# Kernel tuning notes

Measured on AMD Instinct MI355X. Metric: run time of the kernel, lower is better.

The kernel has to match this reference:

```python
import jax, jax.numpy as jnp
import numpy as np

N_NODES = 100000
N_EDGES = 1600000
NFEAT, NHID, NCLASS = 64, 128, 32


def _glorot(key, shape):
    fan_in, fan_out = shape[0], shape[1]
    lim = np.sqrt(6.0 / (fan_in + fan_out))
    return jax.random.uniform(key, shape, jnp.float32, -lim, lim)


def setup_inputs() -> dict:
    key = jax.random.key(0)
    ks = jax.random.split(key, 12)
    x = jax.random.normal(ks[0], (N_NODES, NFEAT), jnp.float32)
    edge_idx = jax.random.randint(ks[1], (2, N_EDGES), 0, N_NODES, jnp.int64)
    edge_weight = jax.random.uniform(ks[2], (N_EDGES,), jnp.float32)
    return {
        "x": x,
        "edge_idx": edge_idx,
        "edge_weight": edge_weight,
        # SAGEConv 1: out = mean_agg(x) @ Wl1 + b1 + x @ Wr1
        "Wl1": _glorot(ks[3], (NFEAT, NHID)),
        "Wr1": _glorot(ks[4], (NFEAT, NHID)),
        "b1": jnp.zeros((NHID,), jnp.float32),
        # SAGEConv 2
        "Wl2": _glorot(ks[5], (NHID, NHID)),
        "Wr2": _glorot(ks[6], (NHID, NHID)),
        "b2": jnp.zeros((NHID,), jnp.float32),
        # fc head: Linear(nhid, nclass) -> Linear(nclass, 1)
        "Wfc1": _glorot(ks[7], (NHID, NCLASS)),
        "bfc1": jnp.zeros((NCLASS,), jnp.float32),
        "Wfc2": _glorot(ks[8], (NCLASS, 1)),
        "bfc2": jnp.zeros((1,), jnp.float32),
    }


def _sage_conv(x, src, dst, Wl, Wr, b, n_nodes):
    # mean aggregation of source features at destination nodes
    msg_sum = jax.ops.segment_sum(x[src], dst, num_segments=n_nodes)  # [N, d]
    deg = jax.ops.segment_sum(jnp.ones((src.shape[0], 1), x.dtype), dst,
                              num_segments=n_nodes)                    # [N, 1]
    mean = msg_sum / jnp.maximum(deg, 1.0)
    return mean @ Wl + b + x @ Wr


def reference(x, edge_idx, edge_weight, Wl1, Wr1, b1, Wl2, Wr2, b2,
              Wfc1, bfc1, Wfc2, bfc2):
    n_nodes = x.shape[0]
    src, dst = edge_idx[0], edge_idx[1]
    # dropout is identity in eval mode (training=False)
    h = _sage_conv(x, src, dst, Wl1, Wr1, b1, n_nodes)   # [N, nhid]
    h = _sage_conv(h, src, dst, Wl2, Wr2, b2, n_nodes)   # [N, nhid]
    h = h @ Wfc1 + bfc1                                   # [N, nclass]
    out = h @ Wfc2 + bfc2                                 # [N, 1]
    return out
```

## Files before the change

### kernel.cpp

```cpp
#include <hip/hip_runtime.h>

#define S_SHIFT 8
#define S_NODES 256
#define NBKT    400
#define CAP     5120
#define CHUNK   8192
#define NREP    8
#define FTH     512
#define NDOTS   160

__global__ __launch_bounds__(FTH) void fused_kernel(
    const float* __restrict__ x,
    const int* __restrict__ src, const int* __restrict__ dst,
    int E, int N, int B, int nscat,
    int* __restrict__ cursor, unsigned* __restrict__ bucket,
    const float* __restrict__ Wl1, const float* __restrict__ Wr1, const float* __restrict__ b1,
    const float* __restrict__ Wl2, const float* __restrict__ Wr2, const float* __restrict__ b2,
    const float* __restrict__ Wfc1, const float* __restrict__ bfc1,
    const float* __restrict__ Wfc2, const float* __restrict__ bfc2,
    float* __restrict__ ga, float2* __restrict__ gbc, float* __restrict__ c01)
{
    __shared__ int hist[NBKT], lbase[NBKT], lcur[NBKT];
    __shared__ float wv[192], uu[128], vl2[128], vr2[128], w2[32];
    int t = threadIdx.x;
    int l = t & 63;
    int w = t >> 6;

    if ((int)blockIdx.x < nscat) {
        int e0 = blockIdx.x * CHUNK;
        int cnt = E - e0; if (cnt > CHUNK) cnt = CHUNK;
        for (int i = t; i < B; i += FTH) hist[i] = 0;
        __syncthreads();
        for (int i = t; i < cnt; i += FTH)
            atomicAdd(&hist[dst[e0 + i] >> S_SHIFT], 1);
        __syncthreads();
        for (int i = t; i < B; i += FTH) {
            lcur[i] = 0;
            if (hist[i] > 0) lbase[i] = atomicAdd(&cursor[i], hist[i]);
        }
        __syncthreads();
        for (int i = t; i < cnt; i += FTH) {
            int d = dst[e0 + i], s = src[e0 + i];
            int bb = d >> S_SHIFT;
            int off = atomicAdd(&lcur[bb], 1);
            bucket[(size_t)bb * CAP + (unsigned)(lbase[bb] + off)] =
                ((unsigned)s << S_SHIFT) | (unsigned)(d & (S_NODES - 1));
        }
    } else {
        if (t < 32) w2[t] = Wfc2[t];
        __syncthreads();
        for (int j = 0; j < 16; ++j) {
            int i = w + 8 * j;
            float p = (l < 32) ? Wfc1[i * 32 + l] * w2[l] : 0.f;
            for (int m = 16; m; m >>= 1) p += __shfl_xor(p, m);
            if (l == 0) uu[i] = p;
        }
        __syncthreads();
        for (int j = 0; j < 16; ++j) {
            int i = w + 8 * j;
            float ua = uu[l], ub = uu[64 + l];
            float pa = Wl2[i * 128 + l] * ua + Wl2[i * 128 + 64 + l] * ub;
            float pb = Wr2[i * 128 + l] * ua + Wr2[i * 128 + 64 + l] * ub;
            for (int m = 32; m; m >>= 1) { pa += __shfl_xor(pa, m); pb += __shfl_xor(pb, m); }
            if (l == 0) { vl2[i] = pa; vr2[i] = pb; }
        }
        __syncthreads();
        for (int j = 0; j < 8; ++j) {
            int i = w + 8 * j;
            float l1a = Wl1[i * 128 + l], l1b = Wl1[i * 128 + 64 + l];
            float r1a = Wr1[i * 128 + l], r1b = Wr1[i * 128 + 64 + l];
            float La = vl2[l], Lb = vl2[64 + l], Ra = vr2[l], Rb = vr2[64 + l];
            float pc = l1a * La + l1b * Lb;
            float pb = l1a * Ra + l1b * Rb + r1a * La + r1b * Lb;
            float pa = r1a * Ra + r1b * Rb;
            for (int m = 32; m; m >>= 1) {
                pa += __shfl_xor(pa, m); pb += __shfl_xor(pb, m); pc += __shfl_xor(pc, m);
            }
            if (l == 0) { wv[i] = pa; wv[64 + i] = pb; wv[128 + i] = pc; }
        }
        if ((int)blockIdx.x == nscat && w == 7) {
            float p0 = b1[l] * vr2[l] + b1[64 + l] * vr2[64 + l]
                     + b2[l] * uu[l] + b2[64 + l] * uu[64 + l];
            if (l < 32) p0 += bfc1[l] * w2[l];
            float p1 = b1[l] * vl2[l] + b1[64 + l] * vl2[64 + l];
            for (int m = 32; m; m >>= 1) { p0 += __shfl_xor(p0, m); p1 += __shfl_xor(p1, m); }
            if (l == 0) { c01[0] = p0 + bfc2[0]; c01[1] = p1; }
        }
        __syncthreads();

        int fp = l & 15, sub = l >> 4;
        float4 wa4 = ((const float4*)wv)[fp];
        float4 wb4 = ((const float4*)wv)[16 + fp];
        float4 wc4 = ((const float4*)wv)[32 + fp];
        const float4* x4 = (const float4*)x;
        int Q = (N + 3) >> 2;
        for (int qd = ((int)blockIdx.x - nscat) * 8 + w; qd < Q; qd += NDOTS * 8) {
            int node = qd * 4 + sub;
            float a = 0.f, b = 0.f, c = 0.f;
            if (node < N) {
                float4 v = x4[(size_t)node * 16 + fp];
                a = v.x * wa4.x + v.y * wa4.y + v.z * wa4.z + v.w * wa4.w;
                b = v.x * wb4.x + v.y * wb4.y + v.z * wb4.z + v.w * wb4.w;
                c = v.x * wc4.x + v.y * wc4.y + v.z * wc4.z + v.w * wc4.w;
            }
            for (int m = 8; m; m >>= 1) {
                a += __shfl_xor(a, m); b += __shfl_xor(b, m); c += __shfl_xor(c, m);
            }
            if (fp == 0 && node < N) { ga[node] = a; gbc[node] = make_float2(b, c); }
        }
    }
}

__global__ __launch_bounds__(512) void aggA_kernel(
    const unsigned* __restrict__ bucket, const int* __restrict__ cursor,
    const float2* __restrict__ gbc, const float* __restrict__ ga,
    const float* __restrict__ c01,
    float* __restrict__ q, float* __restrict__ t1, float* __restrict__ inv, int N)
{
    __shared__ float aB[NREP][S_NODES], aC[NREP][S_NODES];
    __shared__ int cnt[NREP][S_NODES];
    int t = threadIdx.x, b = blockIdx.x;
    int r = t >> 6;
    float* aBf = (float*)aB; float* aCf = (float*)aC; int* cnf = (int*)cnt;
    for (int i = t; i < NREP * S_NODES; i += 512) { aBf[i] = 0.f; aCf[i] = 0.f; cnf[i] = 0; }
    __syncthreads();
    int n = cursor[b];
    const unsigned* bp = bucket + (size_t)b * CAP;
    int n4 = n & ~3;
    for (int i = 4 * t; i < n4; i += 4 * 512) {
        uint4 e4 = *(const uint4*)(bp + i);
        float2 g0 = gbc[e4.x >> S_SHIFT];
        float2 g1 = gbc[e4.y >> S_SHIFT];
        float2 g2 = gbc[e4.z >> S_SHIFT];
        float2 g3 = gbc[e4.w >> S_SHIFT];
        int d0 = e4.x & (S_NODES - 1), d1 = e4.y & (S_NODES - 1);
        int d2 = e4.z & (S_NODES - 1), d3 = e4.w & (S_NODES - 1);
        atomicAdd(&aB[r][d0], g0.x); atomicAdd(&aC[r][d0], g0.y); atomicAdd(&cnt[r][d0], 1);
        atomicAdd(&aB[r][d1], g1.x); atomicAdd(&aC[r][d1], g1.y); atomicAdd(&cnt[r][d1], 1);
        atomicAdd(&aB[r][d2], g2.x); atomicAdd(&aC[r][d2], g2.y); atomicAdd(&cnt[r][d2], 1);
        atomicAdd(&aB[r][d3], g3.x); atomicAdd(&aC[r][d3], g3.y); atomicAdd(&cnt[r][d3], 1);
    }
    if (n4 + t < n) {
        unsigned uu = bp[n4 + t];
        float2 g = gbc[uu >> S_SHIFT];
        int dl = uu & (S_NODES - 1);
        atomicAdd(&aB[r][dl], g.x); atomicAdd(&aC[r][dl], g.y); atomicAdd(&cnt[r][dl], 1);
    }
    __syncthreads();
    if (t < S_NODES) {
        int node = (b << S_SHIFT) + t;
        if (node < N) {
            float sb = 0.f, sc = 0.f; int d = 0;
            #pragma unroll
            for (int k = 0; k < NREP; ++k) { sb += aB[k][t]; sc += aC[k][t]; d += cnt[k][t]; }
            float iv = 1.0f / ((d > 0) ? (float)d : 1.0f);
            inv[node] = iv;
            q[node]   = iv * sc;
            t1[node]  = ga[node] + iv * sb + c01[0] + (d > 0 ? c01[1] : 0.f);
        }
    }
}

__global__ __launch_bounds__(512) void aggB_kernel(
    const unsigned* __restrict__ bucket, const int* __restrict__ cursor,
    const float* __restrict__ q, const float* __restrict__ t1,
    const float* __restrict__ inv, float* __restrict__ out, int N)
{
    __shared__ float a2[NREP][S_NODES];
    int t = threadIdx.x, b = blockIdx.x;
    int r = t >> 6;
    float* a2f = (float*)a2;
    for (int i = t; i < NREP * S_NODES; i += 512) a2f[i] = 0.f;
    __syncthreads();
    int n = cursor[b];
    const unsigned* bp = bucket + (size_t)b * CAP;
    int n4 = n & ~3;
    for (int i = 4 * t; i < n4; i += 4 * 512) {
        uint4 e4 = *(const uint4*)(bp + i);
        float q0 = q[e4.x >> S_SHIFT], q1 = q[e4.y >> S_SHIFT];
        float q2 = q[e4.z >> S_SHIFT], q3 = q[e4.w >> S_SHIFT];
        atomicAdd(&a2[r][e4.x & (S_NODES - 1)], q0);
        atomicAdd(&a2[r][e4.y & (S_NODES - 1)], q1);
        atomicAdd(&a2[r][e4.z & (S_NODES - 1)], q2);
        atomicAdd(&a2[r][e4.w & (S_NODES - 1)], q3);
    }
    if (n4 + t < n) {
        unsigned uu = bp[n4 + t];
        atomicAdd(&a2[r][uu & (S_NODES - 1)], q[uu >> S_SHIFT]);
    }
    __syncthreads();
    if (t < S_NODES) {
        int node = (b << S_SHIFT) + t;
        if (node < N) {
            float s2 = 0.f;
            #pragma unroll
            for (int k = 0; k < NREP; ++k) s2 += a2[k][t];
            out[node] = t1[node] + inv[node] * s2;
        }
    }
}

extern "C" void kernel_launch(void* const* d_in, const int* in_sizes, int n_in,
                              void* d_out, int out_size, void* d_ws, size_t ws_size,
                              hipStream_t stream) {
    const float* x    = (const float*)d_in[0];
    const int*   eidx = (const int*)d_in[1];
    const float* Wl1  = (const float*)d_in[3];
    const float* Wr1  = (const float*)d_in[4];
    const float* b1   = (const float*)d_in[5];
    const float* Wl2  = (const float*)d_in[6];
    const float* Wr2  = (const float*)d_in[7];
    const float* b2   = (const float*)d_in[8];
    const float* Wfc1 = (const float*)d_in[9];
    const float* bfc1 = (const float*)d_in[10];
    const float* Wfc2 = (const float*)d_in[11];
    const float* bfc2 = (const float*)d_in[12];

    const int N = in_sizes[0] / 64;
    const int E = in_sizes[2];
    const int* src = eidx;
    const int* dst = eidx + E;
    const int B = (N + S_NODES - 1) / S_NODES;
    const int nscat = (E + CHUNK - 1) / CHUNK;

    char* ws = (char*)d_ws;
    int*      cursor = (int*)(ws);
    float*    c01    = (float*)(ws + 2048);
    float*    ga     = (float*)(ws + 4096);
    float*    q      = (float*)(ws + 4096 + (size_t)N * 4);
    float*    t1     = (float*)(ws + 4096 + (size_t)N * 8);
    float*    inv    = (float*)(ws + 4096 + (size_t)N * 12);
    float2*   gbc    = (float2*)(ws + 4096 + (size_t)N * 16);
    unsigned* bucket = (unsigned*)(ws + 4096 + (size_t)N * 24);

    hipMemsetAsync(cursor, 0, 2048, stream);

    fused_kernel<<<nscat + NDOTS, FTH, 0, stream>>>(
        x, src, dst, E, N, B, nscat, cursor, bucket,
        Wl1, Wr1, b1, Wl2, Wr2, b2, Wfc1, bfc1, Wfc2, bfc2,
        ga, gbc, c01);

    aggA_kernel<<<B, 512, 0, stream>>>(bucket, cursor, gbc, ga, c01, q, t1, inv, N);
    aggB_kernel<<<B, 512, 0, stream>>>(bucket, cursor, q, t1, inv, (float*)d_out, N);
}
```

Before: 168.7 us.

## Split weight folding into prep kernel and shrink buckets for more parallel blocks

Moves the weight-collapsing math and the cursor zeroing into a single-block prep kernel that writes folded vectors to global memory, replacing the memset and the redundant per-block recomputation in the dot blocks. The bucket granularity drops to 128 nodes, chunks to 4096 edges, replicas to 4, and blocks to 256 threads, so the scatter and aggregation grids have roughly twice as many blocks. The aim is better load balance and occupancy. The cost is an extra serial single-block launch and more global cursor atomics.

```diff
diff --git a/kernel.cpp b/kernel.cpp
--- a/kernel.cpp
+++ b/kernel.cpp
@@ -1,45 +1,97 @@
 #include <hip/hip_runtime.h>
 
-#define S_SHIFT 8
-#define S_NODES 256
-#define NBKT    400
-#define CAP     5120
-#define CHUNK   8192
-#define NREP    8
-#define FTH     512
-#define NDOTS   160
-
-__global__ __launch_bounds__(FTH) void fused_kernel(
-    const float* __restrict__ x,
-    const int* __restrict__ src, const int* __restrict__ dst,
-    int E, int N, int B, int nscat,
-    int* __restrict__ cursor, unsigned* __restrict__ bucket,
+#define S_SHIFT 7
+#define S_NODES 128
+#define NBKT    784
+#define CAP     2560
+#define CHUNK   4096
+#define NREP    4
+#define TPB     256
+#define TOTAL_BLOCKS 1024
+
+__global__ __launch_bounds__(512) void prep_kernel(
     const float* __restrict__ Wl1, const float* __restrict__ Wr1, const float* __restrict__ b1,
     const float* __restrict__ Wl2, const float* __restrict__ Wr2, const float* __restrict__ b2,
     const float* __restrict__ Wfc1, const float* __restrict__ bfc1,
     const float* __restrict__ Wfc2, const float* __restrict__ bfc2,
-    float* __restrict__ ga, float2* __restrict__ gbc, float* __restrict__ c01)
-{
-    __shared__ int hist[NBKT], lbase[NBKT], lcur[NBKT];
+    int* __restrict__ cursor, float* __restrict__ wv_g, float* __restrict__ c01)
+{
     __shared__ float wv[192], uu[128], vl2[128], vr2[128], w2[32];
     int t = threadIdx.x;
     int l = t & 63;
     int w = t >> 6;
-
-    if ((int)blockIdx.x < nscat) {
-        int e0 = blockIdx.x * CHUNK;
+    for (int i = t; i < NBKT; i += 512) cursor[i] = 0;
+    if (t < 32) w2[t] = Wfc2[t];
+    __syncthreads();
+    for (int j = 0; j < 16; ++j) {
+        int i = w + 8 * j;
+        float p = (l < 32) ? Wfc1[i * 32 + l] * w2[l] : 0.f;
+        for (int m = 16; m; m >>= 1) p += __shfl_xor(p, m);
+        if (l == 0) uu[i] = p;
+    }
+    __syncthreads();
+    for (int j = 0; j < 16; ++j) {
+        int i = w + 8 * j;
+        float ua = uu[l], ub = uu[64 + l];
+        float pa = Wl2[i * 128 + l] * ua + Wl2[i * 128 + 64 + l] * ub;
+        float pb = Wr2[i * 128 + l] * ua + Wr2[i * 128 + 64 + l] * ub;
+        for (int m = 32; m; m >>= 1) { pa += __shfl_xor(pa, m); pb += __shfl_xor(pb, m); }
+        if (l == 0) { vl2[i] = pa; vr2[i] = pb; }
+    }
+    __syncthreads();
+    for (int j = 0; j < 8; ++j) {
+        int i = w + 8 * j;
+        float l1a = Wl1[i * 128 + l], l1b = Wl1[i * 128 + 64 + l];
+        float r1a = Wr1[i * 128 + l], r1b = Wr1[i * 128 + 64 + l];
+        float La = vl2[l], Lb = vl2[64 + l], Ra = vr2[l], Rb = vr2[64 + l];
+        float pc = l1a * La + l1b * Lb;
+        float pb = l1a * Ra + l1b * Rb + r1a * La + r1b * Lb;
+        float pa = r1a * Ra + r1b * Rb;
+        for (int m = 32; m; m >>= 1) {
+            pa += __shfl_xor(pa, m); pb += __shfl_xor(pb, m); pc += __shfl_xor(pc, m);
+        }
+        if (l == 0) { wv[i] = pa; wv[64 + i] = pb; wv[128 + i] = pc; }
+    }
+    if (w == 7) {
+        float p0 = b1[l] * vr2[l] + b1[64 + l] * vr2[64 + l]
+                 + b2[l] * uu[l] + b2[64 + l] * uu[64 + l];
+        if (l < 32) p0 += bfc1[l] * w2[l];
+        float p1 = b1[l] * vl2[l] + b1[64 + l] * vl2[64 + l];
+        for (int m = 32; m; m >>= 1) { p0 += __shfl_xor(p0, m); p1 += __shfl_xor(p1, m); }
+        if (l == 0) { c01[0] = p0 + bfc2[0]; c01[1] = p1; }
+    }
+    __syncthreads();
+    for (int i = t; i < 192; i += 512) wv_g[i] = wv[i];
+}
+
+__global__ __launch_bounds__(TPB) void fused_kernel(
+    const float* __restrict__ x,
+    const int* __restrict__ src, const int* __restrict__ dst,
+    int E, int N, int B, int nscat, int ndot,
+    int* __restrict__ cursor, unsigned* __restrict__ bucket,
+    const float* __restrict__ wv_g,
+    float* __restrict__ ga, float2* __restrict__ gbc)
+{
+    __shared__ int hist[NBKT], lbase[NBKT], lcur[NBKT];
+    int t = threadIdx.x;
+    int l = t & 63;
+    int w = t >> 6;
+    int bid = blockIdx.x;
+
+    if (bid < nscat) {
+        int e0 = bid * CHUNK;
         int cnt = E - e0; if (cnt > CHUNK) cnt = CHUNK;
-        for (int i = t; i < B; i += FTH) hist[i] = 0;
+        for (int i = t; i < B; i += TPB) hist[i] = 0;
         __syncthreads();
-        for (int i = t; i < cnt; i += FTH)
+        for (int i = t; i < cnt; i += TPB)
             atomicAdd(&hist[dst[e0 + i] >> S_SHIFT], 1);
         __syncthreads();
-        for (int i = t; i < B; i += FTH) {
+        for (int i = t; i < B; i += TPB) {
             lcur[i] = 0;
             if (hist[i] > 0) lbase[i] = atomicAdd(&cursor[i], hist[i]);
         }
         __syncthreads();
-        for (int i = t; i < cnt; i += FTH) {
+        for (int i = t; i < cnt; i += TPB) {
             int d = dst[e0 + i], s = src[e0 + i];
             int bb = d >> S_SHIFT;
             int off = atomicAdd(&lcur[bb], 1);
@@ -47,54 +99,15 @@
                 ((unsigned)s << S_SHIFT) | (unsigned)(d & (S_NODES - 1));
         }
     } else {
-        if (t < 32) w2[t] = Wfc2[t];
-        __syncthreads();
-        for (int j = 0; j < 16; ++j) {
-            int i = w + 8 * j;
-            float p = (l < 32) ? Wfc1[i * 32 + l] * w2[l] : 0.f;
-            for (int m = 16; m; m >>= 1) p += __shfl_xor(p, m);
-            if (l == 0) uu[i] = p;
-        }
-        __syncthreads();
-        for (int j = 0; j < 16; ++j) {
-            int i = w + 8 * j;
-            float ua = uu[l], ub = uu[64 + l];
-            float pa = Wl2[i * 128 + l] * ua + Wl2[i * 128 + 64 + l] * ub;
-            float pb = Wr2[i * 128 + l] * ua + Wr2[i * 128 + 64 + l] * ub;
-            for (int m = 32; m; m >>= 1) { pa += __shfl_xor(pa, m); pb += __shfl_xor(pb, m); }
-            if (l == 0) { vl2[i] = pa; vr2[i] = pb; }
-        }
-        __syncthreads();
-        for (int j = 0; j < 8; ++j) {
-            int i = w + 8 * j;
-            float l1a = Wl1[i * 128 + l], l1b = Wl1[i * 128 + 64 + l];
-            float r1a = Wr1[i * 128 + l], r1b = Wr1[i * 128 + 64 + l];
-            float La = vl2[l], Lb = vl2[64 + l], Ra = vr2[l], Rb = vr2[64 + l];
-            float pc = l1a * La + l1b * Lb;
-            float pb = l1a * Ra + l1b * Rb + r1a * La + r1b * Lb;
-            float pa = r1a * Ra + r1b * Rb;
-            for (int m = 32; m; m >>= 1) {
-                pa += __shfl_xor(pa, m); pb += __shfl_xor(pb, m); pc += __shfl_xor(pc, m);
-            }
-            if (l == 0) { wv[i] = pa; wv[64 + i] = pb; wv[128 + i] = pc; }
-        }
-        if ((int)blockIdx.x == nscat && w == 7) {
-            float p0 = b1[l] * vr2[l] + b1[64 + l] * vr2[64 + l]
-                     + b2[l] * uu[l] + b2[64 + l] * uu[64 + l];
-            if (l < 32) p0 += bfc1[l] * w2[l];
-            float p1 = b1[l] * vl2[l] + b1[64 + l] * vl2[64 + l];
-            for (int m = 32; m; m >>= 1) { p0 += __shfl_xor(p0, m); p1 += __shfl_xor(p1, m); }
-            if (l == 0) { c01[0] = p0 + bfc2[0]; c01[1] = p1; }
-        }
-        __syncthreads();
-
         int fp = l & 15, sub = l >> 4;
-        float4 wa4 = ((const float4*)wv)[fp];
-        float4 wb4 = ((const float4*)wv)[16 + fp];
-        float4 wc4 = ((const float4*)wv)[32 + fp];
+        float4 wa4 = ((const float4*)wv_g)[fp];
+        float4 wb4 = ((const float4*)wv_g)[16 + fp];
+        float4 wc4 = ((const float4*)wv_g)[32 + fp];
         const float4* x4 = (const float4*)x;
         int Q = (N + 3) >> 2;
-        for (int qd = ((int)blockIdx.x - nscat) * 8 + w; qd < Q; qd += NDOTS * 8) {
+        int wid = (bid - nscat) * (TPB / 64) + w;
+        int stride = ndot * (TPB / 64);
+        for (int qd = wid; qd < Q; qd += stride) {
             int node = qd * 4 + sub;
             float a = 0.f, b = 0.f, c = 0.f;
             if (node < N) {
@@ -111,7 +124,7 @@
     }
 }
 
-__global__ __launch_bounds__(512) void aggA_kernel(
+__global__ __launch_bounds__(TPB) void aggA_kernel(
     const unsigned* __restrict__ bucket, const int* __restrict__ cursor,
     const float2* __restrict__ gbc, const float* __restrict__ ga,
     const float* __restrict__ c01,
@@ -122,12 +135,12 @@
     int t = threadIdx.x, b = blockIdx.x;
     int r = t >> 6;
     float* aBf = (float*)aB; float* aCf = (float*)aC; int* cnf = (int*)cnt;
-    for (int i = t; i < NREP * S_NODES; i += 512) { aBf[i] = 0.f; aCf[i] = 0.f; cnf[i] = 0; }
+    for (int i = t; i < NREP * S_NODES; i += TPB) { aBf[i] = 0.f; aCf[i] = 0.f; cnf[i] = 0; }
     __syncthreads();
     int n = cursor[b];
     const unsigned* bp = bucket + (size_t)b * CAP;
     int n4 = n & ~3;
-    for (int i = 4 * t; i < n4; i += 4 * 512) {
+    for (int i = 4 * t; i < n4; i += 4 * TPB) {
         uint4 e4 = *(const uint4*)(bp + i);
         float2 g0 = gbc[e4.x >> S_SHIFT];
         float2 g1 = gbc[e4.y >> S_SHIFT];
@@ -161,7 +174,7 @@
     }
 }
 
-__global__ __launch_bounds__(512) void aggB_kernel(
+__global__ __launch_bounds__(TPB) void aggB_kernel(
     const unsigned* __restrict__ bucket, const int* __restrict__ cursor,
     const float* __restrict__ q, const float* __restrict__ t1,
     const float* __restrict__ inv, float* __restrict__ out, int N)
@@ -170,12 +183,12 @@
     int t = threadIdx.x, b = blockIdx.x;
     int r = t >> 6;
     float* a2f = (float*)a2;
-    for (int i = t; i < NREP * S_NODES; i += 512) a2f[i] = 0.f;
+    for (int i = t; i < NREP * S_NODES; i += TPB) a2f[i] = 0.f;
     __syncthreads();
     int n = cursor[b];
     const unsigned* bp = bucket + (size_t)b * CAP;
     int n4 = n & ~3;
-    for (int i = 4 * t; i < n4; i += 4 * 512) {
+    for (int i = 4 * t; i < n4; i += 4 * TPB) {
         uint4 e4 = *(const uint4*)(bp + i);
         float q0 = q[e4.x >> S_SHIFT], q1 = q[e4.y >> S_SHIFT];
         float q2 = q[e4.z >> S_SHIFT], q3 = q[e4.w >> S_SHIFT];
@@ -220,12 +233,14 @@
     const int E = in_sizes[2];
     const int* src = eidx;
     const int* dst = eidx + E;
-    const int B = (N + S_NODES - 1) / S_NODES;
+    const int B = (N + S_NODES - 1) >> S_SHIFT;
     const int nscat = (E + CHUNK - 1) / CHUNK;
+    const int ndot = TOTAL_BLOCKS - nscat;
 
     char* ws = (char*)d_ws;
     int*      cursor = (int*)(ws);
-    float*    c01    = (float*)(ws + 2048);
+    float*    wv_g   = (float*)(ws + 3136);
+    float*    c01    = (float*)(ws + 3904);
     float*    ga     = (float*)(ws + 4096);
     float*    q      = (float*)(ws + 4096 + (size_t)N * 4);
     float*    t1     = (float*)(ws + 4096 + (size_t)N * 8);
@@ -233,13 +248,12 @@
     float2*   gbc    = (float2*)(ws + 4096 + (size_t)N * 16);
     unsigned* bucket = (unsigned*)(ws + 4096 + (size_t)N * 24);
 
-    hipMemsetAsync(cursor, 0, 2048, stream);
-
-    fused_kernel<<<nscat + NDOTS, FTH, 0, stream>>>(
-        x, src, dst, E, N, B, nscat, cursor, bucket,
-        Wl1, Wr1, b1, Wl2, Wr2, b2, Wfc1, bfc1, Wfc2, bfc2,
-        ga, gbc, c01);
-
-    aggA_kernel<<<B, 512, 0, stream>>>(bucket, cursor, gbc, ga, c01, q, t1, inv, N);
-    aggB_kernel<<<B, 512, 0, stream>>>(bucket, cursor, q, t1, inv, (float*)d_out, N);
-}
+    prep_kernel<<<1, 512, 0, stream>>>(Wl1, Wr1, b1, Wl2, Wr2, b2,
+                                       Wfc1, bfc1, Wfc2, bfc2, cursor, wv_g, c01);
+
+    fused_kernel<<<TOTAL_BLOCKS, TPB, 0, stream>>>(
+        x, src, dst, E, N, B, nscat, ndot, cursor, bucket, wv_g, ga, gbc);
+
+    aggA_kernel<<<B, TPB, 0, stream>>>(bucket, cursor, gbc, ga, c01, q, t1, inv, N);
+    aggB_kernel<<<B, TPB, 0, stream>>>(bucket, cursor, q, t1, inv, (float*)d_out, N);
+}
```

After: 182.3 us. 8.1% more time.

## Split each bucket's edge aggregation across two blocks and add finalize kernel

Applied to the files above, without the earlier changes.

The edge list of each destination bucket is now processed by two blocks in both aggregation passes, doubling the grid from about 391 to 782 blocks so the GPU's compute units are filled better. Partial sums from the first pass go to separate per-half arrays and are combined in a new finalize kernel that writes q, inv and the base output. The second pass adds its halves into the output with global atomics. This costs an extra kernel launch, more workspace traffic, and non-deterministic float summation order.

```diff
diff --git a/kernel.cpp b/kernel.cpp
--- a/kernel.cpp
+++ b/kernel.cpp
@@ -21,7 +21,8 @@
     float* __restrict__ ga, float2* __restrict__ gbc, float* __restrict__ c01)
 {
     __shared__ int hist[NBKT], lbase[NBKT], lcur[NBKT];
-    __shared__ float wv[192], uu[128], vl2[128], vr2[128], w2[32];
+    __shared__ __align__(16) float wv[192];
+    __shared__ float uu[128], vl2[128], vr2[128], w2[32];
     int t = threadIdx.x;
     int l = t & 63;
     int w = t >> 6;
@@ -113,21 +114,27 @@
 
 __global__ __launch_bounds__(512) void aggA_kernel(
     const unsigned* __restrict__ bucket, const int* __restrict__ cursor,
-    const float2* __restrict__ gbc, const float* __restrict__ ga,
-    const float* __restrict__ c01,
-    float* __restrict__ q, float* __restrict__ t1, float* __restrict__ inv, int N)
+    const float2* __restrict__ gbc,
+    float* __restrict__ sB0, float* __restrict__ sC0, int* __restrict__ cnt0,
+    float* __restrict__ sB1, float* __restrict__ sC1, int* __restrict__ cnt1, int N)
 {
     __shared__ float aB[NREP][S_NODES], aC[NREP][S_NODES];
     __shared__ int cnt[NREP][S_NODES];
-    int t = threadIdx.x, b = blockIdx.x;
+    int t = threadIdx.x, blk = blockIdx.x;
+    int b = blk >> 1, hi = blk & 1;
     int r = t >> 6;
     float* aBf = (float*)aB; float* aCf = (float*)aC; int* cnf = (int*)cnt;
     for (int i = t; i < NREP * S_NODES; i += 512) { aBf[i] = 0.f; aCf[i] = 0.f; cnf[i] = 0; }
     __syncthreads();
     int n = cursor[b];
+    int half = (((n + 1) >> 1) + 3) & ~3;
+    if (half > n) half = n;
+    int start = hi ? half : 0;
+    int end   = hi ? n    : half;
     const unsigned* bp = bucket + (size_t)b * CAP;
-    int n4 = n & ~3;
-    for (int i = 4 * t; i < n4; i += 4 * 512) {
+    int m = end - start;
+    int m4 = m & ~3;
+    for (int i = start + 4 * t; i < start + m4; i += 4 * 512) {
         uint4 e4 = *(const uint4*)(bp + i);
         float2 g0 = gbc[e4.x >> S_SHIFT];
         float2 g1 = gbc[e4.y >> S_SHIFT];
@@ -140,8 +147,9 @@
         atomicAdd(&aB[r][d2], g2.x); atomicAdd(&aC[r][d2], g2.y); atomicAdd(&cnt[r][d2], 1);
         atomicAdd(&aB[r][d3], g3.x); atomicAdd(&aC[r][d3], g3.y); atomicAdd(&cnt[r][d3], 1);
     }
-    if (n4 + t < n) {
-        unsigned uu = bp[n4 + t];
+    int it = start + m4 + t;
+    if (it < end) {
+        unsigned uu = bp[it];
         float2 g = gbc[uu >> S_SHIFT];
         int dl = uu & (S_NODES - 1);
         atomicAdd(&aB[r][dl], g.x); atomicAdd(&aC[r][dl], g.y); atomicAdd(&cnt[r][dl], 1);
@@ -153,29 +161,51 @@
             float sb = 0.f, sc = 0.f; int d = 0;
             #pragma unroll
             for (int k = 0; k < NREP; ++k) { sb += aB[k][t]; sc += aC[k][t]; d += cnt[k][t]; }
-            float iv = 1.0f / ((d > 0) ? (float)d : 1.0f);
-            inv[node] = iv;
-            q[node]   = iv * sc;
-            t1[node]  = ga[node] + iv * sb + c01[0] + (d > 0 ? c01[1] : 0.f);
-        }
+            if (hi == 0) { sB0[node] = sb; sC0[node] = sc; cnt0[node] = d; }
+            else         { sB1[node] = sb; sC1[node] = sc; cnt1[node] = d; }
+        }
+    }
+}
+
+__global__ __launch_bounds__(512) void finalize_kernel(
+    const float* __restrict__ sB0, const float* __restrict__ sC0, const int* __restrict__ cnt0,
+    const float* __restrict__ sB1, const float* __restrict__ sC1, const int* __restrict__ cnt1,
+    const float* __restrict__ ga, const float* __restrict__ c01,
+    float* __restrict__ q, float* __restrict__ inv, float* __restrict__ out, int N)
+{
+    int node = blockIdx.x * 512 + threadIdx.x;
+    if (node < N) {
+        int d = cnt0[node] + cnt1[node];
+        float sb = sB0[node] + sB1[node];
+        float sc = sC0[node] + sC1[node];
+        float iv = 1.0f / ((d > 0) ? (float)d : 1.0f);
+        q[node]   = iv * sc;
+        inv[node] = iv;
+        out[node] = ga[node] + iv * sb + c01[0] + (d > 0 ? c01[1] : 0.f);
     }
 }
 
 __global__ __launch_bounds__(512) void aggB_kernel(
     const unsigned* __restrict__ bucket, const int* __restrict__ cursor,
-    const float* __restrict__ q, const float* __restrict__ t1,
-    const float* __restrict__ inv, float* __restrict__ out, int N)
+    const float* __restrict__ q, const float* __restrict__ inv,
+    float* __restrict__ out, int N)
 {
     __shared__ float a2[NREP][S_NODES];
-    int t = threadIdx.x, b = blockIdx.x;
+    int t = threadIdx.x, blk = blockIdx.x;
+    int b = blk >> 1, hi = blk & 1;
     int r = t >> 6;
     float* a2f = (float*)a2;
     for (int i = t; i < NREP * S_NODES; i += 512) a2f[i] = 0.f;
     __syncthreads();
     int n = cursor[b];
+    int half = (((n + 1) >> 1) + 3) & ~3;
+    if (half > n) half = n;
+    int start = hi ? half : 0;
+    int end   = hi ? n    : half;
     const unsigned* bp = bucket + (size_t)b * CAP;
-    int n4 = n & ~3;
-    for (int i = 4 * t; i < n4; i += 4 * 512) {
+    int m = end - start;
+    int m4 = m & ~3;
+    for (int i = start + 4 * t; i < start + m4; i += 4 * 512) {
         uint4 e4 = *(const uint4*)(bp + i);
         float q0 = q[e4.x >> S_SHIFT], q1 = q[e4.y >> S_SHIFT];
         float q2 = q[e4.z >> S_SHIFT], q3 = q[e4.w >> S_SHIFT];
@@ -184,8 +214,9 @@
         atomicAdd(&a2[r][e4.z & (S_NODES - 1)], q2);
         atomicAdd(&a2[r][e4.w & (S_NODES - 1)], q3);
     }
-    if (n4 + t < n) {
-        unsigned uu = bp[n4 + t];
+    int it = start + m4 + t;
+    if (it < end) {
+        unsigned uu = bp[it];
         atomicAdd(&a2[r][uu & (S_NODES - 1)], q[uu >> S_SHIFT]);
     }
     __syncthreads();
@@ -195,7 +226,7 @@
             float s2 = 0.f;
             #pragma unroll
             for (int k = 0; k < NREP; ++k) s2 += a2[k][t];
-            out[node] = t1[node] + inv[node] * s2;
+            atomicAdd(&out[node], inv[node] * s2);
         }
     }
 }
@@ -220,26 +251,38 @@
     const int E = in_sizes[2];
     const int* src = eidx;
     const int* dst = eidx + E;
-    const int B = (N + S_NODES - 1) / S_NODES;
+    const int B = (N + S_NODES - 1) >> S_SHIFT;
     const int nscat = (E + CHUNK - 1) / CHUNK;
 
     char* ws = (char*)d_ws;
-    int*      cursor = (int*)(ws);
-    float*    c01    = (float*)(ws + 2048);
-    float*    ga     = (float*)(ws + 4096);
-    float*    q      = (float*)(ws + 4096 + (size_t)N * 4);
-    float*    t1     = (float*)(ws + 4096 + (size_t)N * 8);
-    float*    inv    = (float*)(ws + 4096 + (size_t)N * 12);
-    float2*   gbc    = (float2*)(ws + 4096 + (size_t)N * 16);
-    unsigned* bucket = (unsigned*)(ws + 4096 + (size_t)N * 24);
-
-    hipMemsetAsync(cursor, 0, 2048, stream);
+    size_t o = 0;
+    auto take = [&](size_t bytes) { char* p = ws + o; o += (bytes + 127) & ~(size_t)127; return p; };
+    int*      cursor = (int*)take(NBKT * 4);
+    float*    c01    = (float*)take(64);
+    float*    ga     = (float*)take((size_t)N * 4);
+    float*    q      = (float*)take((size_t)N * 4);
+    float*    inv    = (float*)take((size_t)N * 4);
+    float*    sB0    = (float*)take((size_t)N * 4);
+    float*    sC0    = (float*)take((size_t)N * 4);
+    int*      cnt0   = (int*)take((size_t)N * 4);
+    float*    sB1    = (float*)take((size_t)N * 4);
+    float*    sC1    = (float*)take((size_t)N * 4);
+    int*      cnt1   = (int*)take((size_t)N * 4);
+    float2*   gbc    = (float2*)take((size_t)N * 8);
+    unsigned* bucket = (unsigned*)take((size_t)B * CAP * 4);
+
+    hipMemsetAsync(cursor, 0, NBKT * 4, stream);
 
     fused_kernel<<<nscat + NDOTS, FTH, 0, stream>>>(
         x, src, dst, E, N, B, nscat, cursor, bucket,
         Wl1, Wr1, b1, Wl2, Wr2, b2, Wfc1, bfc1, Wfc2, bfc2,
         ga, gbc, c01);
 
-    aggA_kernel<<<B, 512, 0, stream>>>(bucket, cursor, gbc, ga, c01, q, t1, inv, N);
-    aggB_kernel<<<B, 512, 0, stream>>>(bucket, cursor, q, t1, inv, (float*)d_out, N);
-}
+    aggA_kernel<<<2 * B, 512, 0, stream>>>(bucket, cursor, gbc,
+                                           sB0, sC0, cnt0, sB1, sC1, cnt1, N);
+
+    finalize_kernel<<<(N + 511) / 512, 512, 0, stream>>>(
+        sB0, sC0, cnt0, sB1, sC1, cnt1, ga, c01, q, inv, (float*)d_out, N);
+
+    aggB_kernel<<<2 * B, 512, 0, stream>>>(bucket, cursor, q, inv, (float*)d_out, N);
+}
```

Result: slower. 172.5 us (+2.3%).
